# Kernel optimization log

Hardware: AMD Instinct MI355X
Metric: run time of the kernel (lower is better)

## Reference

```python
import jax, jax.numpy as jnp
import numpy as np

H = 16
D_MODEL = 1024
D_K = D_MODEL // H


def setup_inputs() -> dict:
    key = jax.random.key(0)
    ks = jax.random.split(key, 12)
    B, S = 2, 2048
    scale = 1.0 / np.sqrt(D_MODEL)
    inp = {
        "query": jax.random.normal(ks[0], (B, S, D_MODEL), jnp.float32),
        "key": jax.random.normal(ks[1], (B, S, D_MODEL), jnp.float32),
        "value": jax.random.normal(ks[2], (B, S, D_MODEL), jnp.float32),
        "mask": jnp.ones((B, 1, S), jnp.int32),
        "Wq": jax.random.normal(ks[3], (D_MODEL, D_MODEL), jnp.float32) * scale,
        "bq": jnp.zeros((D_MODEL,), jnp.float32),
        "Wk": jax.random.normal(ks[4], (D_MODEL, D_MODEL), jnp.float32) * scale,
        "bk": jnp.zeros((D_MODEL,), jnp.float32),
        "Wv": jax.random.normal(ks[5], (D_MODEL, D_MODEL), jnp.float32) * scale,
        "bv": jnp.zeros((D_MODEL,), jnp.float32),
        "Wo": jax.random.normal(ks[6], (D_MODEL, D_MODEL), jnp.float32) * scale,
        "bo": jnp.zeros((D_MODEL,), jnp.float32),
    }
    return inp


def reference(query, key, value, mask, Wq, bq, Wk, bk, Wv, bv, Wo, bo):
    B, S, _ = query.shape
    # QKV projections, split heads: [B, S, D] -> [B, H, S, d_k]
    def proj(x, W, b):
        y = x @ W.T + b
        return y.reshape(B, -1, H, D_K).transpose(0, 2, 1, 3)

    q = proj(query, Wq, bq)
    k = proj(key, Wk, bk)
    v = proj(value, Wv, bv)

    # scaled dot-product attention with full score matrix [B, H, Sq, Sk]
    scores = jnp.einsum("bhqd,bhkd->bhqk", q, k) / np.sqrt(D_K)
    m = mask[:, None, :, :]  # unsqueeze head dim: [B, 1, 1_or_S, S]
    scores = jnp.where(m == 0, jnp.float32(-1e9), scores)
    p_attn = jax.nn.softmax(scores, axis=-1)  # dropout p=0.0 (eval)
    x = jnp.einsum("bhqk,bhkd->bhqd", p_attn, v)

    # merge heads and output projection
    x = x.transpose(0, 2, 1, 3).reshape(B, -1, H * D_K)
    return x @ Wo.T + bo
```

## Files before the change

kernel.cpp:

```cpp
#include <hip/hip_runtime.h>
#include <hip/hip_bf16.h>
#include <stdint.h>

typedef unsigned short us;
typedef __bf16 bf8 __attribute__((ext_vector_type(8)));
typedef float  f4  __attribute__((ext_vector_type(4)));

typedef unsigned int __attribute__((address_space(1))) as1_uint;
typedef unsigned int __attribute__((address_space(3))) as3_uint;

__device__ __forceinline__ void async_ld16(const void* g, void* l) {
    __builtin_amdgcn_global_load_lds((as1_uint*)g, (as3_uint*)l, 16, 0, 0);
}

__device__ __forceinline__ us f2bf(float f) {
    __hip_bfloat16 h = __float2bfloat16(f);
    us u;
    __builtin_memcpy(&u, &h, 2);
    return u;
}

__device__ __forceinline__ float fexp2(float x) {
#if __has_builtin(__builtin_amdgcn_exp2f)
    return __builtin_amdgcn_exp2f(x);
#else
    return exp2f(x);
#endif
}

#define SCALE_Q 0.18033688011112042f

__global__ __launch_bounds__(256)
void convert_all(const float* __restrict__ s0, const float* __restrict__ s1,
                 const float* __restrict__ s2, const float* __restrict__ s3,
                 const float* __restrict__ s4, const float* __restrict__ s5,
                 const float* __restrict__ s6,
                 us* __restrict__ d0, us* __restrict__ d1, us* __restrict__ d2,
                 us* __restrict__ d3, us* __restrict__ d4, us* __restrict__ d5,
                 us* __restrict__ d6)
{
    size_t i4 = (((size_t)blockIdx.x * 256) + threadIdx.x) << 2;
    const float* src; us* dst; size_t off;
    if (i4 < ((size_t)3 << 22)) {
        unsigned seg = (unsigned)(i4 >> 22);
        off = i4 & (((size_t)1 << 22) - 1);
        src = seg == 0 ? s0 : (seg == 1 ? s1 : s2);
        dst = seg == 0 ? d0 : (seg == 1 ? d1 : d2);
    } else {
        size_t j = i4 - ((size_t)3 << 22);
        unsigned seg = (unsigned)(j >> 20);
        off = j & (((size_t)1 << 20) - 1);
        src = seg == 0 ? s3 : (seg == 1 ? s4 : (seg == 2 ? s5 : s6));
        dst = seg == 0 ? d3 : (seg == 1 ? d4 : (seg == 2 ? d5 : d6));
    }
    float4 f = *(const float4*)(src + off);
    ushort4 o;
    o.x = f2bf(f.x); o.y = f2bf(f.y); o.z = f2bf(f.z); o.w = f2bf(f.w);
    *(ushort4*)(dst + off) = o;
}

template<int MODE, int BN>
__device__ __forceinline__
void gemm_body(const us* __restrict__ A, const us* __restrict__ W,
               const float* __restrict__ bias, void* __restrict__ out,
               float scale, int bx, int by)
{
    __shared__ us lA[128 * 32];
    __shared__ us lB[BN * 32];

    const int tid  = threadIdx.x;
    const int wv   = tid >> 6;
    const int lane = tid & 63;
    const int l15  = lane & 15;
    const int quad = lane >> 4;
    const int kq   = quad << 3;
    const int cr   = quad << 2;
    const int srow = lane >> 2;
    const int scol = (lane & 3) << 3;
    const int m0   = by << 7;
    const int n0   = bx * BN;
    constexpr int MJ = (BN == 128) ? 4 : 2;
    const int wm = (BN == 128) ? ((wv >> 1) << 6) : (wv << 5);
    const int wn = (BN == 128) ? ((wv & 1) << 6) : 0;

    f4 acc[4][MJ];
    const f4 zero = {0.f, 0.f, 0.f, 0.f};
#pragma unroll
    for (int i = 0; i < 4; ++i)
#pragma unroll
        for (int j = 0; j < MJ; ++j) acc[i][j] = zero;

    for (int kt = 0; kt < 1024; kt += 32) {
#pragma unroll
        for (int s = 0; s < 2; ++s) {
            const int chunk = wv * 2 + s;
            const int row   = chunk * 16 + srow;
            async_ld16(A + (size_t)(m0 + row) * 1024 + kt + scol, &lA[chunk * 512]);
        }
        if (BN == 128) {
#pragma unroll
            for (int s = 0; s < 2; ++s) {
                const int chunk = wv * 2 + s;
                const int row   = chunk * 16 + srow;
                async_ld16(W + (size_t)(n0 + row) * 1024 + kt + scol, &lB[chunk * 512]);
            }
        } else {
            const int row = wv * 16 + srow;
            async_ld16(W + (size_t)(n0 + row) * 1024 + kt + scol, &lB[wv * 512]);
        }
        __syncthreads();

        bf8 wf[4], xf[MJ];
#pragma unroll
        for (int i = 0; i < 4; ++i)
            wf[i] = *(const bf8*)&lB[(wn + i * 16 + l15) * 32 + kq];
#pragma unroll
        for (int j = 0; j < MJ; ++j)
            xf[j] = *(const bf8*)&lA[(wm + j * 16 + l15) * 32 + kq];
#pragma unroll
        for (int i = 0; i < 4; ++i)
#pragma unroll
            for (int j = 0; j < MJ; ++j)
                acc[i][j] = __builtin_amdgcn_mfma_f32_16x16x32_bf16(wf[i], xf[j], acc[i][j], 0, 0, 0);
        __syncthreads();
    }

    if (MODE == 2) {
        us* o = (us*)out;
#pragma unroll
        for (int j = 0; j < MJ; ++j) {
            const int f = m0 + wm + j * 16 + l15;
            const float bf_ = bias[f];
            const int hh = f >> 6, dd = f & 63;
#pragma unroll
            for (int i = 0; i < 4; ++i) {
                const int tokb = n0 + wn + i * 16 + cr;
                const int bb = tokb >> 11, ss = tokb & 2047;
                us hp[4];
#pragma unroll
                for (int r = 0; r < 4; ++r) hp[r] = f2bf(acc[i][j][r] + bf_);
                uint2 w;
                w.x = (unsigned)hp[0] | ((unsigned)hp[1] << 16);
                w.y = (unsigned)hp[2] | ((unsigned)hp[3] << 16);
                *(uint2*)&o[((size_t)((bb * 16 + hh) * 64 + dd) << 11) + ss] = w;
            }
        }
        return;
    }

#pragma unroll
    for (int i = 0; i < 4; ++i) {
        const int gnb = n0 + wn + i * 16 + cr;
        const f4 bj = *(const f4*)&bias[gnb];
        if (MODE == 0) {
            us* o = (us*)out;
            const int hh = gnb >> 6, dd = gnb & 63;
#pragma unroll
            for (int j = 0; j < MJ; ++j) {
                const int gm = m0 + wm + j * 16 + l15;
                const int bb = gm >> 11, ss = gm & 2047;
                us hp[4];
#pragma unroll
                for (int r = 0; r < 4; ++r)
                    hp[r] = f2bf((acc[i][j][r] + bj[r]) * scale);
                uint2 w;
                w.x = (unsigned)hp[0] | ((unsigned)hp[1] << 16);
                w.y = (unsigned)hp[2] | ((unsigned)hp[3] << 16);
                *(uint2*)&o[(((size_t)(bb * 16 + hh) * 2048 + ss) << 6) + dd] = w;
            }
        } else {
            float* o = (float*)out;
#pragma unroll
            for (int j = 0; j < MJ; ++j) {
                const int gm = m0 + wm + j * 16 + l15;
                f4 v;
#pragma unroll
                for (int r = 0; r < 4; ++r) v[r] = acc[i][j][r] + bj[r];
                *(f4*)&o[((size_t)gm << 10) + gnb] = v;
            }
        }
    }
}

__global__ __launch_bounds__(256)
void gemm_qkv(const us* __restrict__ XQ, const us* __restrict__ XK,
              const us* __restrict__ XV,
              const us* __restrict__ WQ, const us* __restrict__ WK,
              const us* __restrict__ WV,
              const float* __restrict__ bq, const float* __restrict__ bk,
              const float* __restrict__ bv,
              us* __restrict__ QP, us* __restrict__ KP, us* __restrict__ VT)
{
    const int z = blockIdx.z;
    if (z == 2) {
        gemm_body<2, 128>(WV, XV, bv, VT, 1.0f, blockIdx.y, blockIdx.x);
        return;
    }
    const us* A = z == 0 ? XQ : XK;
    const us* W = z == 0 ? WQ : WK;
    const float* b = z == 0 ? bq : bk;
    us* o = z == 0 ? QP : KP;
    const float scale = z == 0 ? SCALE_Q : 1.0f;
    gemm_body<0, 128>(A, W, b, o, scale, blockIdx.x, blockIdx.y);
}

__global__ __launch_bounds__(256)
void gemm_o(const us* __restrict__ A, const us* __restrict__ W,
            const float* __restrict__ bias, float* __restrict__ out)
{
    gemm_body<1, 64>(A, W, bias, out, 1.0f, blockIdx.x, blockIdx.y);
}

__global__ __launch_bounds__(128)
void flash_attn(const us* __restrict__ Qp, const us* __restrict__ Kp,
                const us* __restrict__ Vtp, const int* __restrict__ maskp,
                us* __restrict__ ctx)
{
    __shared__ us lK[64 * 64];
    __shared__ us lVt[64 * 64];
    __shared__ us lP[2 * 64 * 72];
    __shared__ float lmask[64];

    const int tid  = threadIdx.x;
    const int wv   = tid >> 6;
    const int lane = tid & 63;
    const int l15  = lane & 15;
    const int quad = lane >> 4;
    const int cr   = quad << 2;
    const int l7   = l15 & 7;

    const int q0 = blockIdx.x << 7;
    const int h  = blockIdx.y;
    const int b  = blockIdx.z;

    const size_t headoff = ((size_t)(b * 16 + h)) << 17;
    const us* Qh  = Qp  + headoff;
    const us* Kh  = Kp  + headoff;
    const us* Vth = Vtp + headoff;

    bf8 qf[4][2];
#pragma unroll
    for (int nt = 0; nt < 4; ++nt)
#pragma unroll
        for (int kb = 0; kb < 2; ++kb)
            qf[nt][kb] = *(const bf8*)(Qh + ((size_t)(q0 + wv * 64 + nt * 16 + l15) << 6)
                                          + kb * 32 + (quad << 3));

    const f4 zero = {0.f, 0.f, 0.f, 0.f};
    f4 of[4][4];
#pragma unroll
    for (int dt = 0; dt < 4; ++dt)
#pragma unroll
        for (int nt = 0; nt < 4; ++nt) of[dt][nt] = zero;
    float li[4] = {0.f, 0.f, 0.f, 0.f};

    us* lPw = lP + wv * (64 * 72);

    const int sr = tid >> 3;
    const int sc = tid & 7;

    for (int kt0 = 0; kt0 < 2048; kt0 += 64) {
        __syncthreads();

#pragma unroll
        for (int it = 0; it < 4; ++it) {
            const int r = sr + 16 * it;
            const int sw = (sc ^ (r & 7)) << 3;
            uint4 kv = *(const uint4*)(Kh + ((size_t)(kt0 + r) << 6) + sc * 8);
            *(uint4*)&lK[(r << 6) + sw] = kv;
            uint4 vv = *(const uint4*)(Vth + (size_t)r * 2048 + kt0 + sc * 8);
            *(uint4*)&lVt[(r << 6) + sw] = vv;
        }
        if (tid < 64)
            lmask[tid] = (maskp[((size_t)b << 11) + kt0 + tid] == 0) ? 0.0f : 1.0f;
        __syncthreads();

        float rs[4] = {0.f, 0.f, 0.f, 0.f};
#pragma unroll
        for (int kt = 0; kt < 4; ++kt) {
            const int krow = (kt * 16 + l15) << 6;
            bf8 kf0 = *(const bf8*)&lK[krow + ((quad ^ l7) << 3)];
            bf8 kf1 = *(const bf8*)&lK[krow + (((4 + quad) ^ l7) << 3)];
            f4 st[4];
#pragma unroll
            for (int nt = 0; nt < 4; ++nt) {
                st[nt] = __builtin_amdgcn_mfma_f32_16x16x32_bf16(kf0, qf[nt][0], zero, 0, 0, 0);
                st[nt] = __builtin_amdgcn_mfma_f32_16x16x32_bf16(kf1, qf[nt][1], st[nt], 0, 0, 0);
            }
            const f4 mr = *(const f4*)&lmask[kt * 16 + cr];
#pragma unroll
            for (int nt = 0; nt < 4; ++nt) {
                us hp[4];
#pragma unroll
                for (int r = 0; r < 4; ++r) {
                    const float p = fexp2(st[nt][r]) * mr[r];
                    rs[nt] += p;
                    hp[r] = f2bf(p);
                }
                uint2 w;
                w.x = (unsigned)hp[0] | ((unsigned)hp[1] << 16);
                w.y = (unsigned)hp[2] | ((unsigned)hp[3] << 16);
                *(uint2*)&lPw[(nt * 16 + l15) * 72 + kt * 16 + cr] = w;
            }
        }
#pragma unroll
        for (int nt = 0; nt < 4; ++nt) {
            float r2 = rs[nt];
            r2 += __shfl_xor(r2, 16, 64);
            r2 += __shfl_xor(r2, 32, 64);
            li[nt] += r2;
        }

#pragma unroll
        for (int kb = 0; kb < 2; ++kb) {
            bf8 pfr[4];
#pragma unroll
            for (int nt = 0; nt < 4; ++nt)
                pfr[nt] = *(const bf8*)&lPw[(nt * 16 + l15) * 72 + kb * 32 + (quad << 3)];
#pragma unroll
            for (int dt = 0; dt < 4; ++dt) {
                bf8 vf = *(const bf8*)&lVt[((dt * 16 + l15) << 6) + (((kb * 4 + quad) ^ l7) << 3)];
#pragma unroll
                for (int nt = 0; nt < 4; ++nt)
                    of[dt][nt] = __builtin_amdgcn_mfma_f32_16x16x32_bf16(vf, pfr[nt], of[dt][nt], 0, 0, 0);
            }
        }
    }

#pragma unroll
    for (int nt = 0; nt < 4; ++nt) {
        const float linv = 1.0f / li[nt];
        const int tok = q0 + wv * 64 + nt * 16 + l15;
        const size_t rowb = (((size_t)(b * 2048 + tok)) << 10) + (h << 6);
#pragma unroll
        for (int dt = 0; dt < 4; ++dt) {
            us hp[4];
#pragma unroll
            for (int r = 0; r < 4; ++r) hp[r] = f2bf(of[dt][nt][r] * linv);
            uint2 w;
            w.x = (unsigned)hp[0] | ((unsigned)hp[1] << 16);
            w.y = (unsigned)hp[2] | ((unsigned)hp[3] << 16);
            *(uint2*)&ctx[rowb + dt * 16 + cr] = w;
        }
    }
}

extern "C" void kernel_launch(void* const* d_in, const int* in_sizes, int n_in,
                              void* d_out, int out_size, void* d_ws, size_t ws_size,
                              hipStream_t stream)
{
    const float* q    = (const float*)d_in[0];
    const float* k    = (const float*)d_in[1];
    const float* v    = (const float*)d_in[2];
    const int*   mask = (const int*)d_in[3];
    const float* Wq   = (const float*)d_in[4];
    const float* bq   = (const float*)d_in[5];
    const float* Wk   = (const float*)d_in[6];
    const float* bk   = (const float*)d_in[7];
    const float* Wv   = (const float*)d_in[8];
    const float* bv   = (const float*)d_in[9];
    const float* Wo   = (const float*)d_in[10];
    const float* bo   = (const float*)d_in[11];
    float* out = (float*)d_out;

    us* ws  = (us*)d_ws;
    us* XQ  = ws;
    us* XK  = ws + 4194304;
    us* XV  = ws + 8388608;
    us* WQb = ws + 12582912;
    us* WKb = ws + 13631488;
    us* WVb = ws + 14680064;
    us* WOb = ws + 15728640;
    us* QP  = ws + 16777216;
    us* KP  = ws + 20971520;
    us* VT  = ws + 25165824;
    us* CTX = XQ;

    convert_all<<<16384, 256, 0, stream>>>(q, k, v, Wq, Wk, Wv, Wo,
                                           XQ, XK, XV, WQb, WKb, WVb, WOb);
    gemm_qkv<<<dim3(8, 32, 3), 256, 0, stream>>>(XQ, XK, XV, WQb, WKb, WVb,
                                                 bq, bk, bv, QP, KP, VT);
    flash_attn<<<dim3(16, 16, 2), 128, 0, stream>>>(QP, KP, VT, mask, CTX);
    gemm_o<<<dim3(16, 32), 256, 0, stream>>>(CTX, WOb, bo, out);
}
```

Before: 257.0 us.

## Double-buffer LDS tiles with async global-to-LDS loads in GEMM and attention

Both the GEMM body and the flash-attention kernel now keep two LDS buffers. The next K-tile is issued with async global_load_lds while MFMA work runs on the current buffer, which removes one barrier per iteration and is meant to hide global-load latency. In attention, the XOR swizzle moves from the LDS store address to the global source column so that async loads can fill it. The LDS mask staging is dropped in favour of direct int4 mask reads from global memory. The cost is double the LDS footprint, which may lower occupancy, and extra global mask reads per tile.

```diff
diff --git a/kernel.cpp b/kernel.cpp
--- a/kernel.cpp
+++ b/kernel.cpp
@@ -65,8 +65,8 @@
                const float* __restrict__ bias, void* __restrict__ out,
                float scale, int bx, int by)
 {
-    __shared__ us lA[128 * 32];
-    __shared__ us lB[BN * 32];
+    __shared__ us lA[2][128 * 32];
+    __shared__ us lB[2][BN * 32];
 
     const int tid  = threadIdx.x;
     const int wv   = tid >> 6;
@@ -90,33 +90,40 @@
 #pragma unroll
         for (int j = 0; j < MJ; ++j) acc[i][j] = zero;
 
-    for (int kt = 0; kt < 1024; kt += 32) {
+    auto issue = [&](int kt, int bb) {
 #pragma unroll
         for (int s = 0; s < 2; ++s) {
             const int chunk = wv * 2 + s;
             const int row   = chunk * 16 + srow;
-            async_ld16(A + (size_t)(m0 + row) * 1024 + kt + scol, &lA[chunk * 512]);
+            async_ld16(A + (size_t)(m0 + row) * 1024 + kt + scol, &lA[bb][chunk * 512]);
         }
         if (BN == 128) {
 #pragma unroll
             for (int s = 0; s < 2; ++s) {
                 const int chunk = wv * 2 + s;
                 const int row   = chunk * 16 + srow;
-                async_ld16(W + (size_t)(n0 + row) * 1024 + kt + scol, &lB[chunk * 512]);
+                async_ld16(W + (size_t)(n0 + row) * 1024 + kt + scol, &lB[bb][chunk * 512]);
             }
         } else {
             const int row = wv * 16 + srow;
-            async_ld16(W + (size_t)(n0 + row) * 1024 + kt + scol, &lB[wv * 512]);
-        }
-        __syncthreads();
+            async_ld16(W + (size_t)(n0 + row) * 1024 + kt + scol, &lB[bb][wv * 512]);
+        }
+    };
+
+    issue(0, 0);
+    __syncthreads();
+
+    for (int kt = 0; kt < 1024; kt += 32) {
+        const int bb = (kt >> 5) & 1;
+        if (kt + 32 < 1024) issue(kt + 32, bb ^ 1);
 
         bf8 wf[4], xf[MJ];
 #pragma unroll
         for (int i = 0; i < 4; ++i)
-            wf[i] = *(const bf8*)&lB[(wn + i * 16 + l15) * 32 + kq];
+            wf[i] = *(const bf8*)&lB[bb][(wn + i * 16 + l15) * 32 + kq];
 #pragma unroll
         for (int j = 0; j < MJ; ++j)
-            xf[j] = *(const bf8*)&lA[(wm + j * 16 + l15) * 32 + kq];
+            xf[j] = *(const bf8*)&lA[bb][(wm + j * 16 + l15) * 32 + kq];
 #pragma unroll
         for (int i = 0; i < 4; ++i)
 #pragma unroll
@@ -135,14 +142,14 @@
 #pragma unroll
             for (int i = 0; i < 4; ++i) {
                 const int tokb = n0 + wn + i * 16 + cr;
-                const int bb = tokb >> 11, ss = tokb & 2047;
+                const int bb2 = tokb >> 11, ss = tokb & 2047;
                 us hp[4];
 #pragma unroll
                 for (int r = 0; r < 4; ++r) hp[r] = f2bf(acc[i][j][r] + bf_);
                 uint2 w;
                 w.x = (unsigned)hp[0] | ((unsigned)hp[1] << 16);
                 w.y = (unsigned)hp[2] | ((unsigned)hp[3] << 16);
-                *(uint2*)&o[((size_t)((bb * 16 + hh) * 64 + dd) << 11) + ss] = w;
+                *(uint2*)&o[((size_t)((bb2 * 16 + hh) * 64 + dd) << 11) + ss] = w;
             }
         }
         return;
@@ -158,7 +165,7 @@
 #pragma unroll
             for (int j = 0; j < MJ; ++j) {
                 const int gm = m0 + wm + j * 16 + l15;
-                const int bb = gm >> 11, ss = gm & 2047;
+                const int bb2 = gm >> 11, ss = gm & 2047;
                 us hp[4];
 #pragma unroll
                 for (int r = 0; r < 4; ++r)
@@ -166,7 +173,7 @@
                 uint2 w;
                 w.x = (unsigned)hp[0] | ((unsigned)hp[1] << 16);
                 w.y = (unsigned)hp[2] | ((unsigned)hp[3] << 16);
-                *(uint2*)&o[(((size_t)(bb * 16 + hh) * 2048 + ss) << 6) + dd] = w;
+                *(uint2*)&o[(((size_t)(bb2 * 16 + hh) * 2048 + ss) << 6) + dd] = w;
             }
         } else {
             float* o = (float*)out;
@@ -216,10 +223,9 @@
                 const us* __restrict__ Vtp, const int* __restrict__ maskp,
                 us* __restrict__ ctx)
 {
-    __shared__ us lK[64 * 64];
-    __shared__ us lVt[64 * 64];
+    __shared__ us lK[2][64 * 64];
+    __shared__ us lVt[2][64 * 64];
     __shared__ us lP[2 * 64 * 72];
-    __shared__ float lmask[64];
 
     const int tid  = threadIdx.x;
     const int wv   = tid >> 6;
@@ -228,6 +234,8 @@
     const int quad = lane >> 4;
     const int cr   = quad << 2;
     const int l7   = l15 & 7;
+    const int r8   = lane >> 3;
+    const int c8   = lane & 7;
 
     const int q0 = blockIdx.x << 7;
     const int h  = blockIdx.y;
@@ -237,6 +245,7 @@
     const us* Qh  = Qp  + headoff;
     const us* Kh  = Kp  + headoff;
     const us* Vth = Vtp + headoff;
+    const int* mrow = maskp + ((size_t)b << 11);
 
     bf8 qf[4][2];
 #pragma unroll
@@ -256,38 +265,41 @@
 
     us* lPw = lP + wv * (64 * 72);
 
-    const int sr = tid >> 3;
-    const int sc = tid & 7;
+    auto issue = [&](int kt0n, int bb) {
+#pragma unroll
+        for (int g = 0; g < 4; ++g) {
+            const int R  = wv * 32 + g * 8 + r8;
+            const int cl = (c8 ^ (R & 7)) << 3;
+            async_ld16(Kh + ((size_t)(kt0n + R) << 6) + cl, &lK[bb][(wv * 32 + g * 8) << 6]);
+            async_ld16(Vth + ((size_t)R << 11) + kt0n + cl, &lVt[bb][(wv * 32 + g * 8) << 6]);
+        }
+    };
+
+    issue(0, 0);
+    __syncthreads();
 
     for (int kt0 = 0; kt0 < 2048; kt0 += 64) {
-        __syncthreads();
-
-#pragma unroll
-        for (int it = 0; it < 4; ++it) {
-            const int r = sr + 16 * it;
-            const int sw = (sc ^ (r & 7)) << 3;
-            uint4 kv = *(const uint4*)(Kh + ((size_t)(kt0 + r) << 6) + sc * 8);
-            *(uint4*)&lK[(r << 6) + sw] = kv;
-            uint4 vv = *(const uint4*)(Vth + (size_t)r * 2048 + kt0 + sc * 8);
-            *(uint4*)&lVt[(r << 6) + sw] = vv;
-        }
-        if (tid < 64)
-            lmask[tid] = (maskp[((size_t)b << 11) + kt0 + tid] == 0) ? 0.0f : 1.0f;
-        __syncthreads();
+        const int bb = (kt0 >> 6) & 1;
+        if (kt0 + 64 < 2048) issue(kt0 + 64, bb ^ 1);
 
         float rs[4] = {0.f, 0.f, 0.f, 0.f};
 #pragma unroll
         for (int kt = 0; kt < 4; ++kt) {
             const int krow = (kt * 16 + l15) << 6;
-            bf8 kf0 = *(const bf8*)&lK[krow + ((quad ^ l7) << 3)];
-            bf8 kf1 = *(const bf8*)&lK[krow + (((4 + quad) ^ l7) << 3)];
+            bf8 kf0 = *(const bf8*)&lK[bb][krow + ((quad ^ l7) << 3)];
+            bf8 kf1 = *(const bf8*)&lK[bb][krow + (((4 + quad) ^ l7) << 3)];
             f4 st[4];
 #pragma unroll
             for (int nt = 0; nt < 4; ++nt) {
                 st[nt] = __builtin_amdgcn_mfma_f32_16x16x32_bf16(kf0, qf[nt][0], zero, 0, 0, 0);
                 st[nt] = __builtin_amdgcn_mfma_f32_16x16x32_bf16(kf1, qf[nt][1], st[nt], 0, 0, 0);
             }
-            const f4 mr = *(const f4*)&lmask[kt * 16 + cr];
+            const int4 m4 = *(const int4*)(mrow + kt0 + kt * 16 + cr);
+            f4 mr;
+            mr[0] = m4.x ? 1.0f : 0.0f;
+            mr[1] = m4.y ? 1.0f : 0.0f;
+            mr[2] = m4.z ? 1.0f : 0.0f;
+            mr[3] = m4.w ? 1.0f : 0.0f;
 #pragma unroll
             for (int nt = 0; nt < 4; ++nt) {
                 us hp[4];
@@ -319,12 +331,13 @@
                 pfr[nt] = *(const bf8*)&lPw[(nt * 16 + l15) * 72 + kb * 32 + (quad << 3)];
 #pragma unroll
             for (int dt = 0; dt < 4; ++dt) {
-                bf8 vf = *(const bf8*)&lVt[((dt * 16 + l15) << 6) + (((kb * 4 + quad) ^ l7) << 3)];
+                bf8 vf = *(const bf8*)&lVt[bb][((dt * 16 + l15) << 6) + (((kb * 4 + quad) ^ l7) << 3)];
 #pragma unroll
                 for (int nt = 0; nt < 4; ++nt)
                     of[dt][nt] = __builtin_amdgcn_mfma_f32_16x16x32_bf16(vf, pfr[nt], of[dt][nt], 0, 0, 0);
             }
         }
+        __syncthreads();
     }
 
 #pragma unroll
```

Result: slower. 285.3 us (+11.0%).

## Split flash attention query tile across four waves and use packed bf16 conversion

Applied to the files above, without the earlier changes.

The flash attention block goes from two waves of 64 query rows each to four waves of 32 rows each, so the same 128-row tile is spread over more waves. This halves per-wave accumulator registers, which should allow more waves in flight, and each wave now loads its own slice of the K/V tile. The mask is read straight from global memory as int4 instead of being staged in LDS. Float-to-bf16 packing throughout uses the paired __float22bfloat162_rn conversion in place of scalar conversions plus shifts. The trade-off is that K/V fragments in LDS are now re-read by more waves per query row.

```diff
diff --git a/kernel.cpp b/kernel.cpp
--- a/kernel.cpp
+++ b/kernel.cpp
@@ -17,6 +17,13 @@
     __hip_bfloat16 h = __float2bfloat16(f);
     us u;
     __builtin_memcpy(&u, &h, 2);
+    return u;
+}
+
+__device__ __forceinline__ unsigned pack2bf(float a, float b) {
+    __hip_bfloat162 h2 = __float22bfloat162_rn(make_float2(a, b));
+    unsigned u;
+    __builtin_memcpy(&u, &h2, 4);
     return u;
 }
 
@@ -135,14 +142,11 @@
 #pragma unroll
             for (int i = 0; i < 4; ++i) {
                 const int tokb = n0 + wn + i * 16 + cr;
-                const int bb = tokb >> 11, ss = tokb & 2047;
-                us hp[4];
-#pragma unroll
-                for (int r = 0; r < 4; ++r) hp[r] = f2bf(acc[i][j][r] + bf_);
+                const int bb2 = tokb >> 11, ss = tokb & 2047;
                 uint2 w;
-                w.x = (unsigned)hp[0] | ((unsigned)hp[1] << 16);
-                w.y = (unsigned)hp[2] | ((unsigned)hp[3] << 16);
-                *(uint2*)&o[((size_t)((bb * 16 + hh) * 64 + dd) << 11) + ss] = w;
+                w.x = pack2bf(acc[i][j][0] + bf_, acc[i][j][1] + bf_);
+                w.y = pack2bf(acc[i][j][2] + bf_, acc[i][j][3] + bf_);
+                *(uint2*)&o[((size_t)((bb2 * 16 + hh) * 64 + dd) << 11) + ss] = w;
             }
         }
         return;
@@ -158,15 +162,11 @@
 #pragma unroll
             for (int j = 0; j < MJ; ++j) {
                 const int gm = m0 + wm + j * 16 + l15;
-                const int bb = gm >> 11, ss = gm & 2047;
-                us hp[4];
-#pragma unroll
-                for (int r = 0; r < 4; ++r)
-                    hp[r] = f2bf((acc[i][j][r] + bj[r]) * scale);
+                const int bb2 = gm >> 11, ss = gm & 2047;
                 uint2 w;
-                w.x = (unsigned)hp[0] | ((unsigned)hp[1] << 16);
-                w.y = (unsigned)hp[2] | ((unsigned)hp[3] << 16);
-                *(uint2*)&o[(((size_t)(bb * 16 + hh) * 2048 + ss) << 6) + dd] = w;
+                w.x = pack2bf((acc[i][j][0] + bj[0]) * scale, (acc[i][j][1] + bj[1]) * scale);
+                w.y = pack2bf((acc[i][j][2] + bj[2]) * scale, (acc[i][j][3] + bj[3]) * scale);
+                *(uint2*)&o[(((size_t)(bb2 * 16 + hh) * 2048 + ss) << 6) + dd] = w;
             }
         } else {
             float* o = (float*)out;
@@ -211,15 +211,14 @@
     gemm_body<1, 64>(A, W, bias, out, 1.0f, blockIdx.x, blockIdx.y);
 }
 
-__global__ __launch_bounds__(128)
+__global__ __launch_bounds__(256)
 void flash_attn(const us* __restrict__ Qp, const us* __restrict__ Kp,
                 const us* __restrict__ Vtp, const int* __restrict__ maskp,
                 us* __restrict__ ctx)
 {
     __shared__ us lK[64 * 64];
     __shared__ us lVt[64 * 64];
-    __shared__ us lP[2 * 64 * 72];
-    __shared__ float lmask[64];
+    __shared__ us lP[4 * 32 * 72];
 
     const int tid  = threadIdx.x;
     const int wv   = tid >> 6;
@@ -237,74 +236,76 @@
     const us* Qh  = Qp  + headoff;
     const us* Kh  = Kp  + headoff;
     const us* Vth = Vtp + headoff;
-
-    bf8 qf[4][2];
-#pragma unroll
-    for (int nt = 0; nt < 4; ++nt)
+    const int* mrow = maskp + ((size_t)b << 11);
+
+    bf8 qf[2][2];
+#pragma unroll
+    for (int nt = 0; nt < 2; ++nt)
 #pragma unroll
         for (int kb = 0; kb < 2; ++kb)
-            qf[nt][kb] = *(const bf8*)(Qh + ((size_t)(q0 + wv * 64 + nt * 16 + l15) << 6)
+            qf[nt][kb] = *(const bf8*)(Qh + ((size_t)(q0 + wv * 32 + nt * 16 + l15) << 6)
                                           + kb * 32 + (quad << 3));
 
     const f4 zero = {0.f, 0.f, 0.f, 0.f};
-    f4 of[4][4];
+    f4 of[4][2];
 #pragma unroll
     for (int dt = 0; dt < 4; ++dt)
 #pragma unroll
-        for (int nt = 0; nt < 4; ++nt) of[dt][nt] = zero;
-    float li[4] = {0.f, 0.f, 0.f, 0.f};
-
-    us* lPw = lP + wv * (64 * 72);
-
-    const int sr = tid >> 3;
-    const int sc = tid & 7;
+        for (int nt = 0; nt < 2; ++nt) of[dt][nt] = zero;
+    float li[2] = {0.f, 0.f};
+
+    us* lPw = lP + wv * (32 * 72);
+
+    const int sr = lane >> 3;
+    const int sc = lane & 7;
 
     for (int kt0 = 0; kt0 < 2048; kt0 += 64) {
         __syncthreads();
 
 #pragma unroll
-        for (int it = 0; it < 4; ++it) {
-            const int r = sr + 16 * it;
+        for (int it = 0; it < 2; ++it) {
+            const int r = wv * 16 + it * 8 + sr;
             const int sw = (sc ^ (r & 7)) << 3;
             uint4 kv = *(const uint4*)(Kh + ((size_t)(kt0 + r) << 6) + sc * 8);
             *(uint4*)&lK[(r << 6) + sw] = kv;
-            uint4 vv = *(const uint4*)(Vth + (size_t)r * 2048 + kt0 + sc * 8);
+            uint4 vv = *(const uint4*)(Vth + ((size_t)r << 11) + kt0 + sc * 8);
             *(uint4*)&lVt[(r << 6) + sw] = vv;
         }
-        if (tid < 64)
-            lmask[tid] = (maskp[((size_t)b << 11) + kt0 + tid] == 0) ? 0.0f : 1.0f;
         __syncthreads();
 
-        float rs[4] = {0.f, 0.f, 0.f, 0.f};
+        float rs[2] = {0.f, 0.f};
 #pragma unroll
         for (int kt = 0; kt < 4; ++kt) {
             const int krow = (kt * 16 + l15) << 6;
             bf8 kf0 = *(const bf8*)&lK[krow + ((quad ^ l7) << 3)];
             bf8 kf1 = *(const bf8*)&lK[krow + (((4 + quad) ^ l7) << 3)];
-            f4 st[4];
-#pragma unroll
-            for (int nt = 0; nt < 4; ++nt) {
+            f4 st[2];
+#pragma unroll
+            for (int nt = 0; nt < 2; ++nt) {
                 st[nt] = __builtin_amdgcn_mfma_f32_16x16x32_bf16(kf0, qf[nt][0], zero, 0, 0, 0);
                 st[nt] = __builtin_amdgcn_mfma_f32_16x16x32_bf16(kf1, qf[nt][1], st[nt], 0, 0, 0);
             }
-            const f4 mr = *(const f4*)&lmask[kt * 16 + cr];
-#pragma unroll
-            for (int nt = 0; nt < 4; ++nt) {
-                us hp[4];
-#pragma unroll
-                for (int r = 0; r < 4; ++r) {
-                    const float p = fexp2(st[nt][r]) * mr[r];
-                    rs[nt] += p;
-                    hp[r] = f2bf(p);
-                }
+            const int4 m4 = *(const int4*)(mrow + kt0 + kt * 16 + cr);
+            f4 mr;
+            mr[0] = m4.x ? 1.0f : 0.0f;
+            mr[1] = m4.y ? 1.0f : 0.0f;
+            mr[2] = m4.z ? 1.0f : 0.0f;
+            mr[3] = m4.w ? 1.0f : 0.0f;
+#pragma unroll
+            for (int nt = 0; nt < 2; ++nt) {
+                float p0 = fexp2(st[nt][0]) * mr[0];
+                float p1 = fexp2(st[nt][1]) * mr[1];
+                float p2 = fexp2(st[nt][2]) * mr[2];
+                float p3 = fexp2(st[nt][3]) * mr[3];
+                rs[nt] += (p0 + p1) + (p2 + p3);
                 uint2 w;
-                w.x = (unsigned)hp[0] | ((unsigned)hp[1] << 16);
-                w.y = (unsigned)hp[2] | ((unsigned)hp[3] << 16);
+                w.x = pack2bf(p0, p1);
+                w.y = pack2bf(p2, p3);
                 *(uint2*)&lPw[(nt * 16 + l15) * 72 + kt * 16 + cr] = w;
             }
         }
 #pragma unroll
-        for (int nt = 0; nt < 4; ++nt) {
+        for (int nt = 0; nt < 2; ++nt) {
             float r2 = rs[nt];
             r2 += __shfl_xor(r2, 16, 64);
             r2 += __shfl_xor(r2, 32, 64);
@@ -313,33 +314,30 @@
 
 #pragma unroll
         for (int kb = 0; kb < 2; ++kb) {
-            bf8 pfr[4];
-#pragma unroll
-            for (int nt = 0; nt < 4; ++nt)
+            bf8 pfr[2];
+#pragma unroll
+            for (int nt = 0; nt < 2; ++nt)
                 pfr[nt] = *(const bf8*)&lPw[(nt * 16 + l15) * 72 + kb * 32 + (quad << 3)];
 #pragma unroll
             for (int dt = 0; dt < 4; ++dt) {
                 bf8 vf = *(const bf8*)&lVt[((dt * 16 + l15) << 6) + (((kb * 4 + quad) ^ l7) << 3)];
 #pragma unroll
-                for (int nt = 0; nt < 4; ++nt)
+                for (int nt = 0; nt < 2; ++nt)
                     of[dt][nt] = __builtin_amdgcn_mfma_f32_16x16x32_bf16(vf, pfr[nt], of[dt][nt], 0, 0, 0);
             }
         }
     }
 
 #pragma unroll
-    for (int nt = 0; nt < 4; ++nt) {
+    for (int nt = 0; nt < 2; ++nt) {
         const float linv = 1.0f / li[nt];
-        const int tok = q0 + wv * 64 + nt * 16 + l15;
+        const int tok = q0 + wv * 32 + nt * 16 + l15;
         const size_t rowb = (((size_t)(b * 2048 + tok)) << 10) + (h << 6);
 #pragma unroll
         for (int dt = 0; dt < 4; ++dt) {
-            us hp[4];
-#pragma unroll
-            for (int r = 0; r < 4; ++r) hp[r] = f2bf(of[dt][nt][r] * linv);
             uint2 w;
-            w.x = (unsigned)hp[0] | ((unsigned)hp[1] << 16);
-            w.y = (unsigned)hp[2] | ((unsigned)hp[3] << 16);
+            w.x = pack2bf(of[dt][nt][0] * linv, of[dt][nt][1] * linv);
+            w.y = pack2bf(of[dt][nt][2] * linv, of[dt][nt][3] * linv);
             *(uint2*)&ctx[rowb + dt * 16 + cr] = w;
         }
     }
@@ -380,6 +378,6 @@
                                            XQ, XK, XV, WQb, WKb, WVb, WOb);
     gemm_qkv<<<dim3(8, 32, 3), 256, 0, stream>>>(XQ, XK, XV, WQb, WKb, WVb,
                                                  bq, bk, bv, QP, KP, VT);
-    flash_attn<<<dim3(16, 16, 2), 128, 0, stream>>>(QP, KP, VT, mask, CTX);
+    flash_attn<<<dim3(16, 16, 2), 256, 0, stream>>>(QP, KP, VT, mask, CTX);
     gemm_o<<<dim3(16, 32), 256, 0, stream>>>(CTX, WOb, bo, out);
 }
```

Measured after the change: 283.7 us. 1.1x slower.
